# Kernel tuning notes

Hardware: AMD Instinct MI355X
Metric: run time of the kernel (lower is better)

Reference implementation:

```python
import jax, jax.numpy as jnp
import numpy as np

B, T, C = 16, 2048, 384
E = 8          # num_experts
TOP_K = 2
CAP_F = 1.0
D_FF = 4 * C   # 1536


def setup_inputs() -> dict:
    key = jax.random.key(0)
    ks = jax.random.split(key, 10)
    s = 0.02
    return {
        "x": jax.random.normal(ks[0], (B, T, C), dtype=jnp.float32),
        "noise": jax.random.normal(ks[1], (B, T, E), dtype=jnp.float32),
        "w_route": jax.random.normal(ks[2], (C, E), dtype=jnp.float32) * s,
        "b_route": jnp.zeros((E,), dtype=jnp.float32),
        "w_noise": jax.random.normal(ks[3], (C, E), dtype=jnp.float32) * s,
        "b_noise": jnp.zeros((E,), dtype=jnp.float32),
        "w1": jax.random.normal(ks[4], (E, C, D_FF), dtype=jnp.float32) * s,
        "b1": jnp.zeros((E, D_FF), dtype=jnp.float32),
        "w2": jax.random.normal(ks[5], (E, D_FF, C), dtype=jnp.float32) * s,
        "b2": jnp.zeros((E, C), dtype=jnp.float32),
    }


def _moe_forward(x, noise, w_route, b_route, w_noise, b_noise, w1, b1, w2, b2):
    Bx, Tx, Cx = x.shape
    N = Bx * Tx
    cap = int(N * TOP_K / E * CAP_F)  # static expert capacity

    # --- NoisyTopkRouter ---
    logits = jnp.einsum('btc,ce->bte', x, w_route) + b_route
    noise_logits = jnp.einsum('btc,ce->bte', x, w_noise) + b_noise
    noisy = logits + noise * jax.nn.softplus(noise_logits)
    topv, topi = jax.lax.top_k(noisy, TOP_K)                    # [B,T,K]
    keep_mask = jnp.any(jax.nn.one_hot(topi, E, dtype=jnp.bool_), axis=-2)  # [B,T,E]
    sparse_logits = jnp.where(keep_mask, noisy, -jnp.inf)
    gating = jax.nn.softmax(sparse_logits, axis=-1)             # [B,T,E]

    # --- dispatch by top-1 expert with capacity drop (eval: dropout off) ---
    flat_x = x.reshape(N, Cx)
    flat_g = gating.reshape(N, E)
    top1 = jnp.argmax(flat_g, axis=-1)                          # [N]
    token_ids = jnp.arange(N, dtype=jnp.int32)
    out = jnp.zeros_like(flat_x)

    for i in range(E):
        mask = top1 == i                                        # [N]
        pos = jnp.cumsum(mask) - 1                              # rank within expert
        keep = mask & (pos < cap)
        slot = jnp.where(keep, pos, cap)                        # overflow -> dummy slot
        buf = jnp.zeros((cap + 1,), dtype=jnp.int32).at[slot].set(token_ids)
        idx = buf[:cap]                                         # token id per capacity slot
        valid = (jnp.arange(cap) < jnp.sum(keep))[:, None]      # [cap,1]
        xi = flat_x[idx]                                        # [cap,C] gather
        h = jnp.square(jax.nn.relu(xi @ w1[i] + b1[i]))         # ReLU^2
        yi = h @ w2[i] + b2[i]                                  # [cap,C]
        weighted = yi * flat_g[idx, i][:, None] * valid
        out = out.at[idx].add(weighted)                         # scatter-add

    return out.reshape(Bx, Tx, Cx)


def reference(x, noise, w_route, b_route, w_noise, b_noise, w1, b1, w2, b2):
    return _moe_forward(x, noise, w_route, b_route, w_noise, b_noise, w1, b1, w2, b2)
```

## Files before the change

### kernel.cpp

```cpp
#include <hip/hip_runtime.h>
#include <stdint.h>

#define E_NUM 8
#define CAP 8192
#define NTOK 32768
#define CDIM 384
#define DFF 1536
#define CNT_PAD 64

typedef unsigned short u16;
typedef __attribute__((ext_vector_type(8))) short short8;
typedef __attribute__((ext_vector_type(4))) float f32x4;

__device__ inline u16 f2bf(float f) {
    uint32_t u = __builtin_bit_cast(uint32_t, f);
    u += 0x7fffu + ((u >> 16) & 1u);
    return (u16)(u >> 16);
}

__device__ inline void gload_lds16(const void* g, void* l) {
    __builtin_amdgcn_global_load_lds(
        (const __attribute__((address_space(1))) void*)(uintptr_t)g,
        (__attribute__((address_space(3))) void*)(uint32_t)(uintptr_t)l,
        16, 0, 0);
}

__device__ inline float rsum_to_halves(float v) {
    int s;
    s = __builtin_bit_cast(int, v);
    v += __builtin_bit_cast(float, __builtin_amdgcn_update_dpp(0, s, 0x121, 0xF, 0xF, false));
    s = __builtin_bit_cast(int, v);
    v += __builtin_bit_cast(float, __builtin_amdgcn_update_dpp(0, s, 0x122, 0xF, 0xF, false));
    s = __builtin_bit_cast(int, v);
    v += __builtin_bit_cast(float, __builtin_amdgcn_update_dpp(0, s, 0x124, 0xF, 0xF, false));
    s = __builtin_bit_cast(int, v);
    v += __builtin_bit_cast(float, __builtin_amdgcn_update_dpp(0, s, 0x128, 0xF, 0xF, false));
    s = __builtin_bit_cast(int, v);
    v += __builtin_bit_cast(float, __builtin_amdgcn_ds_swizzle(s, 0x401F));
    return v;
}

__device__ inline float lane_total(float v) {
    int s = __builtin_bit_cast(int, v);
    return __builtin_bit_cast(float, __builtin_amdgcn_readlane(s, 0)) +
           __builtin_bit_cast(float, __builtin_amdgcn_readlane(s, 32));
}

__device__ inline void expert_span(const int* __restrict__ cnt, int e,
                                   int& base, int& n_e) {
    base = 0; n_e = 0;
#pragma unroll
    for (int i = 0; i < E_NUM; ++i) {
        int n = min(cnt[i * CNT_PAD], CAP);
        if (i < e) base += (n + 127) & ~127;
        else if (i == e) n_e = n;
    }
}

__global__ __launch_bounds__(256, 1) void routing_kernel(
    const float* __restrict__ x, const float* __restrict__ noise,
    const float* __restrict__ w_route, const float* __restrict__ b_route,
    const float* __restrict__ w_noise, const float* __restrict__ b_noise,
    int* __restrict__ cnt, int* __restrict__ list, float* __restrict__ gate)
{
    __shared__ int s_top1[16];
    int lane = threadIdx.x & 63, w = threadIdx.x >> 6;
    float4 wr4[12], wn4[12];
#pragma unroll
    for (int i = 0; i < 6; ++i) {
        const float4* pr = (const float4*)(w_route + (size_t)(lane + 64 * i) * 8);
        const float4* pn = (const float4*)(w_noise + (size_t)(lane + 64 * i) * 8);
        wr4[2 * i] = pr[0]; wr4[2 * i + 1] = pr[1];
        wn4[2 * i] = pn[0]; wn4[2 * i + 1] = pn[1];
    }
    float br[E_NUM], bn[E_NUM];
#pragma unroll
    for (int e = 0; e < E_NUM; ++e) { br[e] = b_route[e]; bn[e] = b_noise[e]; }

    int tbase = blockIdx.x * 16 + w * 4;
#pragma unroll
    for (int tt = 0; tt < 4; ++tt) {
        int t = tbase + tt;
        const float* xr = x + (size_t)t * CDIM;
        float xv[6];
#pragma unroll
        for (int i = 0; i < 6; ++i) xv[i] = xr[lane + i * 64];
        float ar[E_NUM], an[E_NUM];
#pragma unroll
        for (int e = 0; e < E_NUM; ++e) { ar[e] = 0.f; an[e] = 0.f; }
#pragma unroll
        for (int i = 0; i < 6; ++i) {
            float4 r0 = wr4[2 * i], r1 = wr4[2 * i + 1];
            float4 n0 = wn4[2 * i], n1 = wn4[2 * i + 1];
            float xi = xv[i];
            ar[0] += xi * r0.x; ar[1] += xi * r0.y; ar[2] += xi * r0.z; ar[3] += xi * r0.w;
            ar[4] += xi * r1.x; ar[5] += xi * r1.y; ar[6] += xi * r1.z; ar[7] += xi * r1.w;
            an[0] += xi * n0.x; an[1] += xi * n0.y; an[2] += xi * n0.z; an[3] += xi * n0.w;
            an[4] += xi * n1.x; an[5] += xi * n1.y; an[6] += xi * n1.z; an[7] += xi * n1.w;
        }
        float nz[E_NUM];
        const float* np = noise + (size_t)t * E_NUM;
#pragma unroll
        for (int e = 0; e < E_NUM; ++e) {
            float sr = lane_total(rsum_to_halves(ar[e])) + br[e];
            float sn = lane_total(rsum_to_halves(an[e])) + bn[e];
            float sp = fmaxf(sn, 0.f) + __logf(1.f + __expf(-fabsf(sn)));
            nz[e] = sr + np[e] * sp;
        }
        float v1 = -1e30f; int i1 = 0;
#pragma unroll
        for (int e = 0; e < E_NUM; ++e) if (nz[e] > v1) { v1 = nz[e]; i1 = e; }
        float v2 = -1e30f;
#pragma unroll
        for (int e = 0; e < E_NUM; ++e) if (e != i1 && nz[e] > v2) v2 = nz[e];
        if (lane == 0) {
            gate[t] = 1.f / (1.f + __expf(v2 - v1));
            s_top1[w * 4 + tt] = i1;
        }
    }
    __syncthreads();
    if (w == 0) {
        int tok = blockIdx.x * 16 + lane;
        int e1 = (lane < 16) ? s_top1[lane] : -1;
#pragma unroll
        for (int e = 0; e < E_NUM; ++e) {
            unsigned long long m = __ballot(e1 == e);
            if (m == 0) continue;
            int c = __popcll(m);
            int leader = __ffsll((long long)m) - 1;
            int basec = 0;
            if (lane == leader) basec = atomicAdd(&cnt[e * CNT_PAD], c);
            basec = __shfl(basec, leader);
            if (e1 == e) {
                int pos = basec + __popcll(m & ((1ull << lane) - 1ull));
                if (pos < CAP) list[e * CAP + pos] = tok;
            }
        }
    }
}

__global__ __launch_bounds__(256) void transpose_cvt_kernel(
    const float* __restrict__ w1, u16* __restrict__ W1t,
    const float* __restrict__ w2, u16* __restrict__ W2t)
{
    __shared__ float tile[32][33];
    int z = blockIdx.z;
    const float* in; u16* out; int R, S, r0, c0;
    if (z < E_NUM) {
        in = w1 + (size_t)z * CDIM * DFF;  out = W1t + (size_t)z * CDIM * DFF;
        R = CDIM; S = DFF;
        c0 = blockIdx.x * 32; r0 = blockIdx.y * 32;
    } else {
        in = w2 + (size_t)(z - E_NUM) * DFF * CDIM;
        out = W2t + (size_t)(z - E_NUM) * DFF * CDIM;
        R = DFF; S = CDIM;
        r0 = blockIdx.x * 32; c0 = blockIdx.y * 32;
    }
    int tx = threadIdx.x, ty = threadIdx.y;
#pragma unroll
    for (int i = ty; i < 32; i += 8)
        tile[i][tx] = in[(size_t)(r0 + i) * S + (c0 + tx)];
    __syncthreads();
#pragma unroll
    for (int i = ty; i < 32; i += 8)
        out[(size_t)(c0 + i) * R + (r0 + tx)] = f2bf(tile[tx][i]);
}

__global__ __launch_bounds__(256) void gather_kernel(
    const float* __restrict__ x, const int* __restrict__ list,
    const int* __restrict__ cnt, u16* __restrict__ Xg)
{
    int e = blockIdx.z;
    int base, n_e;
    expert_span(cnt, e, base, n_e);
    int w = threadIdx.x >> 6, lane = threadIdx.x & 63;
    int row = blockIdx.x * 4 + w;
    int pad = (n_e + 127) & ~127;
    if (row >= pad) return;
    uint32_t* orow = (uint32_t*)(Xg + (size_t)(base + row) * CDIM);
    if (row < n_e) {
        const float2* xr = (const float2*)(x + (size_t)list[e * CAP + row] * CDIM);
#pragma unroll
        for (int i = 0; i < CDIM / 128; ++i) {
            float2 v = xr[lane + i * 64];
            orow[lane + i * 64] = (uint32_t)f2bf(v.x) | ((uint32_t)f2bf(v.y) << 16);
        }
    } else {
#pragma unroll
        for (int i = 0; i < CDIM / 128; ++i) orow[lane + i * 64] = 0;
    }
}

template <int KD, int ND, bool FFN1>
__global__ __launch_bounds__(256, 2) void gemm_kernel(
    const u16* __restrict__ A, const u16* __restrict__ Bt,
    const float* __restrict__ bias, u16* __restrict__ H, float* __restrict__ Out,
    const int* __restrict__ cnt, const int* __restrict__ list,
    const float* __restrict__ gate)
{
    constexpr int NT = ND / 128;
    int bid = blockIdx.x;
    int xcd = bid & 7, slot = bid >> 3;
    int n_idx = slot % NT;
    int mglob = xcd + 8 * (slot / NT);
    int e = mglob >> 6;
    int m0 = (mglob & 63) * 128;
    int base, n_e;
    expert_span(cnt, e, base, n_e);
    int pad_e = (n_e + 127) & ~127;
    if (m0 >= pad_e) return;
    const u16* Ae = A + (size_t)(base + m0) * KD;
    const u16* Be = Bt + ((size_t)e * ND + (size_t)n_idx * 128) * KD;

    __shared__ __align__(16) u16 As[2][128 * 64];
    __shared__ __align__(16) u16 Bs[2][128 * 64];

    int tid = threadIdx.x;
    int w = tid >> 6, lane = tid & 63;
    int quad = lane >> 4, l15 = lane & 15;
    int wr = w & 1, wc = w >> 1;

    int srow = tid >> 3;
    int gcol = ((tid & 7) ^ ((tid >> 3) & 7)) * 8;

    auto stage = [&](int buf, int kb) {
#pragma unroll
        for (int i = 0; i < 4; ++i) {
            int row = i * 32 + srow;
            gload_lds16(Ae + (size_t)row * KD + kb * 64 + gcol, &As[buf][i * 2048 + tid * 8]);
            gload_lds16(Be + (size_t)row * KD + kb * 64 + gcol, &Bs[buf][i * 2048 + tid * 8]);
        }
    };

    f32x4 acc[4][4];
    f32x4 zero = {0.f, 0.f, 0.f, 0.f};
#pragma unroll
    for (int a = 0; a < 4; ++a)
#pragma unroll
        for (int b = 0; b < 4; ++b) acc[a][b] = zero;

    constexpr int NK = KD / 64;
    stage(0, 0);
#pragma unroll 2
    for (int kb = 0; kb < NK; ++kb) {
        const int cur = kb & 1;
        if (kb + 1 < NK) {
            stage(cur ^ 1, kb + 1);
            asm volatile("s_waitcnt vmcnt(8)" ::: "memory");
        } else {
            asm volatile("s_waitcnt vmcnt(0)" ::: "memory");
        }
        __builtin_amdgcn_s_barrier();
        __builtin_amdgcn_sched_barrier(0);
#pragma unroll
        for (int h = 0; h < 2; ++h) {
            int pga = (((h * 4 + quad) ^ (l15 & 7))) * 8;
            short8 af[4], bf[4];
#pragma unroll
            for (int t = 0; t < 4; ++t) {
                af[t] = *(const short8*)&As[cur][(wr * 64 + t * 16 + l15) * 64 + pga];
                bf[t] = *(const short8*)&Bs[cur][(wc * 64 + t * 16 + l15) * 64 + pga];
            }
#pragma unroll
            for (int mt = 0; mt < 4; ++mt)
#pragma unroll
                for (int nt = 0; nt < 4; ++nt)
                    acc[mt][nt] = __builtin_amdgcn_mfma_f32_16x16x32_bf16(
                        af[mt], bf[nt], acc[mt][nt], 0, 0, 0);
        }
        __builtin_amdgcn_sched_barrier(0);
        __builtin_amdgcn_s_barrier();
        __builtin_amdgcn_sched_barrier(0);
    }

    int n0 = n_idx * 128;
    if (FFN1) {
        u16* He = H + (size_t)(base + m0) * ND;
#pragma unroll
        for (int mt = 0; mt < 4; ++mt) {
            int rowL = wr * 64 + mt * 16 + quad * 4;
#pragma unroll
            for (int nt = 0; nt < 4; ++nt) {
                int col = n0 + wc * 64 + nt * 16 + l15;
                float b = bias[(size_t)e * ND + col];
#pragma unroll
                for (int r = 0; r < 4; ++r) {
                    float v = acc[mt][nt][r] + b;
                    v = fmaxf(v, 0.f);
                    v = v * v;
                    He[(size_t)(rowL + r) * ND + col] = f2bf(v);
                }
            }
        }
    } else {
#pragma unroll
        for (int mt = 0; mt < 4; ++mt) {
            int rowL = wr * 64 + mt * 16 + quad * 4;
#pragma unroll
            for (int r = 0; r < 4; ++r) {
                int rr = m0 + rowL + r;
                if (rr < n_e) {
                    int tok = list[(size_t)e * CAP + rr];
                    float g = gate[tok];
#pragma unroll
                    for (int nt = 0; nt < 4; ++nt) {
                        int col = n0 + wc * 64 + nt * 16 + l15;
                        float v = acc[mt][nt][r] + bias[(size_t)e * ND + col];
                        Out[(size_t)tok * CDIM + col] = v * g;
                    }
                }
            }
        }
    }
}

extern "C" void kernel_launch(void* const* d_in, const int* in_sizes, int n_in,
                              void* d_out, int out_size, void* d_ws, size_t ws_size,
                              hipStream_t stream)
{
    const float* x       = (const float*)d_in[0];
    const float* noise   = (const float*)d_in[1];
    const float* w_route = (const float*)d_in[2];
    const float* b_route = (const float*)d_in[3];
    const float* w_noise = (const float*)d_in[4];
    const float* b_noise = (const float*)d_in[5];
    const float* w1      = (const float*)d_in[6];
    const float* b1      = (const float*)d_in[7];
    const float* w2      = (const float*)d_in[8];
    const float* b2      = (const float*)d_in[9];
    float* out = (float*)d_out;

    char* ws = (char*)d_ws;
    size_t off = 0;
    auto alloc = [&](size_t bytes) {
        char* p = ws + off;
        off += (bytes + 255) & ~(size_t)255;
        return p;
    };
    int*   cnt  = (int*)alloc((size_t)E_NUM * CNT_PAD * sizeof(int));
    int*   list = (int*)alloc((size_t)E_NUM * CAP * sizeof(int));
    float* gate = (float*)alloc((size_t)NTOK * sizeof(float));
    u16*   W1t  = (u16*)alloc((size_t)E_NUM * DFF * CDIM * 2);
    u16*   W2t  = (u16*)alloc((size_t)E_NUM * CDIM * DFF * 2);

    size_t rows = NTOK + E_NUM * 128;
    u16* Xg = (u16*)alloc(rows * CDIM * 2);
    u16* Hb = (u16*)alloc(rows * DFF * 2);

    hipMemsetAsync(cnt, 0, (size_t)E_NUM * CNT_PAD * sizeof(int), stream);

    routing_kernel<<<NTOK / 16, 256, 0, stream>>>(x, noise, w_route, b_route,
                                                  w_noise, b_noise, cnt, list, gate);
    transpose_cvt_kernel<<<dim3(48, 12, 16), dim3(32, 8), 0, stream>>>(w1, W1t, w2, W2t);
    gather_kernel<<<dim3(CAP / 4, 1, E_NUM), 256, 0, stream>>>(x, list, cnt, Xg);

    gemm_kernel<CDIM, DFF, true><<<dim3((DFF / 128) * 512), 256, 0, stream>>>(
        Xg, W1t, b1, Hb, nullptr, cnt, nullptr, nullptr);
    gemm_kernel<DFF, CDIM, false><<<dim3((CDIM / 128) * 512), 256, 0, stream>>>(
        Hb, W2t, b2, nullptr, out, cnt, list, gate);
}
```

Measured before the change: 313.2 us.

## Fuse token gather into FFN1 GEMM loads and stage H stores through LDS

Removes the separate gather kernel. The routing kernel now also writes a bf16 copy of x, and the first GEMM loads A rows indirectly through a per-block token index table, with padded rows pointing at a zeroed dummy row. The FFN1 epilogue also writes ReLU² results into swizzled LDS and then stores them as coalesced 16-byte vectors, replacing scattered 2-byte stores. The aim is to save one kernel launch and one full read/write pass of the gathered activations. The cost is an extra bf16 write of all tokens during routing, non-contiguous A loads, and extra LDS syncs.

```diff
diff --git a/kernel.cpp b/kernel.cpp
--- a/kernel.cpp
+++ b/kernel.cpp
@@ -61,7 +61,8 @@
     const float* __restrict__ x, const float* __restrict__ noise,
     const float* __restrict__ w_route, const float* __restrict__ b_route,
     const float* __restrict__ w_noise, const float* __restrict__ b_noise,
-    int* __restrict__ cnt, int* __restrict__ list, float* __restrict__ gate)
+    int* __restrict__ cnt, int* __restrict__ list, float* __restrict__ gate,
+    u16* __restrict__ xbf)
 {
     __shared__ int s_top1[16];
     int lane = threadIdx.x & 63, w = threadIdx.x >> 6;
@@ -85,6 +86,9 @@
         float xv[6];
 #pragma unroll
         for (int i = 0; i < 6; ++i) xv[i] = xr[lane + i * 64];
+        u16* xb = xbf + (size_t)t * CDIM;
+#pragma unroll
+        for (int i = 0; i < 6; ++i) xb[lane + i * 64] = f2bf(xv[i]);
         float ar[E_NUM], an[E_NUM];
 #pragma unroll
         for (int e = 0; e < E_NUM; ++e) { ar[e] = 0.f; an[e] = 0.f; }
@@ -164,31 +168,6 @@
 #pragma unroll
     for (int i = ty; i < 32; i += 8)
         out[(size_t)(c0 + i) * R + (r0 + tx)] = f2bf(tile[tx][i]);
-}
-
-__global__ __launch_bounds__(256) void gather_kernel(
-    const float* __restrict__ x, const int* __restrict__ list,
-    const int* __restrict__ cnt, u16* __restrict__ Xg)
-{
-    int e = blockIdx.z;
-    int base, n_e;
-    expert_span(cnt, e, base, n_e);
-    int w = threadIdx.x >> 6, lane = threadIdx.x & 63;
-    int row = blockIdx.x * 4 + w;
-    int pad = (n_e + 127) & ~127;
-    if (row >= pad) return;
-    uint32_t* orow = (uint32_t*)(Xg + (size_t)(base + row) * CDIM);
-    if (row < n_e) {
-        const float2* xr = (const float2*)(x + (size_t)list[e * CAP + row] * CDIM);
-#pragma unroll
-        for (int i = 0; i < CDIM / 128; ++i) {
-            float2 v = xr[lane + i * 64];
-            orow[lane + i * 64] = (uint32_t)f2bf(v.x) | ((uint32_t)f2bf(v.y) << 16);
-        }
-    } else {
-#pragma unroll
-        for (int i = 0; i < CDIM / 128; ++i) orow[lane + i * 64] = 0;
-    }
 }
 
 template <int KD, int ND, bool FFN1>
@@ -209,11 +188,11 @@
     expert_span(cnt, e, base, n_e);
     int pad_e = (n_e + 127) & ~127;
     if (m0 >= pad_e) return;
-    const u16* Ae = A + (size_t)(base + m0) * KD;
     const u16* Be = Bt + ((size_t)e * ND + (size_t)n_idx * 128) * KD;
 
     __shared__ __align__(16) u16 As[2][128 * 64];
     __shared__ __align__(16) u16 Bs[2][128 * 64];
+    __shared__ int s_tok[128];
 
     int tid = threadIdx.x;
     int w = tid >> 6, lane = tid & 63;
@@ -223,12 +202,27 @@
     int srow = tid >> 3;
     int gcol = ((tid & 7) ^ ((tid >> 3) & 7)) * 8;
 
+    if (FFN1) {
+        if (tid < 128) {
+            int rr = m0 + tid;
+            s_tok[tid] = (rr < n_e) ? list[(size_t)e * CAP + rr] : NTOK;
+        }
+        __syncthreads();
+    }
+    const u16* Arow[4];
+#pragma unroll
+    for (int i = 0; i < 4; ++i) {
+        int row = i * 32 + srow;
+        if (FFN1) Arow[i] = A + (size_t)s_tok[row] * KD;
+        else      Arow[i] = A + (size_t)(base + m0 + row) * KD;
+    }
+
     auto stage = [&](int buf, int kb) {
 #pragma unroll
         for (int i = 0; i < 4; ++i) {
-            int row = i * 32 + srow;
-            gload_lds16(Ae + (size_t)row * KD + kb * 64 + gcol, &As[buf][i * 2048 + tid * 8]);
-            gload_lds16(Be + (size_t)row * KD + kb * 64 + gcol, &Bs[buf][i * 2048 + tid * 8]);
+            gload_lds16(Arow[i] + kb * 64 + gcol, &As[buf][i * 2048 + tid * 8]);
+            gload_lds16(Be + (size_t)(i * 32 + srow) * KD + kb * 64 + gcol,
+                        &Bs[buf][i * 2048 + tid * 8]);
         }
     };
 
@@ -275,22 +269,32 @@
 
     int n0 = n_idx * 128;
     if (FFN1) {
-        u16* He = H + (size_t)(base + m0) * ND;
+        u16* Hs = (u16*)&As[0][0];
 #pragma unroll
         for (int mt = 0; mt < 4; ++mt) {
             int rowL = wr * 64 + mt * 16 + quad * 4;
 #pragma unroll
             for (int nt = 0; nt < 4; ++nt) {
-                int col = n0 + wc * 64 + nt * 16 + l15;
-                float b = bias[(size_t)e * ND + col];
+                int colL = wc * 64 + nt * 16 + l15;
+                float b = bias[(size_t)e * ND + n0 + colL];
 #pragma unroll
                 for (int r = 0; r < 4; ++r) {
                     float v = acc[mt][nt][r] + b;
                     v = fmaxf(v, 0.f);
-                    v = v * v;
-                    He[(size_t)(rowL + r) * ND + col] = f2bf(v);
+                    int row = rowL + r;
+                    Hs[row * 128 + (colL ^ ((row & 7) << 3))] = f2bf(v * v);
                 }
             }
+        }
+        __syncthreads();
+        u16* He = H + (size_t)(base + m0) * ND + n0;
+#pragma unroll
+        for (int j = 0; j < 8; ++j) {
+            int idx = tid + j * 256;
+            int row = idx >> 4;
+            int c8 = (idx & 15) * 8;
+            *(f32x4*)(He + (size_t)row * ND + c8) =
+                *(const f32x4*)(Hs + row * 128 + (c8 ^ ((row & 7) << 3)));
         }
     } else {
 #pragma unroll
@@ -343,19 +347,19 @@
     u16*   W1t  = (u16*)alloc((size_t)E_NUM * DFF * CDIM * 2);
     u16*   W2t  = (u16*)alloc((size_t)E_NUM * CDIM * DFF * 2);
 
+    u16* Xbf = (u16*)alloc((size_t)(NTOK + 1) * CDIM * 2);
     size_t rows = NTOK + E_NUM * 128;
-    u16* Xg = (u16*)alloc(rows * CDIM * 2);
     u16* Hb = (u16*)alloc(rows * DFF * 2);
 
     hipMemsetAsync(cnt, 0, (size_t)E_NUM * CNT_PAD * sizeof(int), stream);
+    hipMemsetAsync(Xbf + (size_t)NTOK * CDIM, 0, CDIM * 2, stream);
 
     routing_kernel<<<NTOK / 16, 256, 0, stream>>>(x, noise, w_route, b_route,
-                                                  w_noise, b_noise, cnt, list, gate);
+                                                  w_noise, b_noise, cnt, list, gate, Xbf);
     transpose_cvt_kernel<<<dim3(48, 12, 16), dim3(32, 8), 0, stream>>>(w1, W1t, w2, W2t);
-    gather_kernel<<<dim3(CAP / 4, 1, E_NUM), 256, 0, stream>>>(x, list, cnt, Xg);
 
     gemm_kernel<CDIM, DFF, true><<<dim3((DFF / 128) * 512), 256, 0, stream>>>(
-        Xg, W1t, b1, Hb, nullptr, cnt, nullptr, nullptr);
+        Xbf, W1t, b1, Hb, nullptr, cnt, list, nullptr);
     gemm_kernel<DFF, CDIM, false><<<dim3((CDIM / 128) * 512), 256, 0, stream>>>(
         Hb, W2t, b2, nullptr, out, cnt, list, gate);
 }
```

New measurement: 315.7 us. No clear change (+0.8%).
